# Kernel tuning notes

Measured on AMD Instinct MI355X. Metric: run time of the kernel, lower is better.

Reference implementation:

```python
import jax, jax.numpy as jnp
import numpy as np

B, Q, H, NH, HD = 2, 1024, 2048, 16, 128
QKV_ALPHA = 1e-4   # W8A8B8O8Linear output scale (a)
QKV_BETA = 1.0     # W8A8B8O8Linear bias scale (b)
QK_SCALE = 1e-4    # BMM_S8T_S8N_F32T dequant scale
PV_SCALE = 2e-3    # BMM_S8T_S8N_S8T output scale
DENSE_ALPHA = 1e-5 # W8A8BFP32OFP32Linear dequant scale
INV_NORM = 1.0 / (HD ** 0.5)


def setup_inputs() -> dict:
    key = jax.random.key(0)
    ks = jax.random.split(key, 8)
    hidden_states = jax.random.randint(ks[0], (B, Q, H), -128, 128, dtype=jnp.int32)  # int8 activations
    residual = jax.random.normal(ks[1], (B, Q, H), dtype=jnp.float32)
    alibi = jax.random.normal(ks[2], (B * NH, 1, Q), dtype=jnp.float32) * 0.1
    causal = jnp.triu(jnp.ones((Q, Q), dtype=bool), k=1)  # True = masked (future positions)
    attention_mask = jnp.broadcast_to(causal[None, None], (B, 1, Q, Q))
    w_qkv = jax.random.randint(ks[3], (3 * H, H), -128, 128, dtype=jnp.int32)   # int8 weight
    b_qkv = jax.random.randint(ks[4], (3 * H,), -128, 128, dtype=jnp.int32)     # int8 bias
    w_dense = jax.random.randint(ks[5], (H, H), -128, 128, dtype=jnp.int32)     # int8 weight
    b_dense = jax.random.normal(ks[6], (H,), dtype=jnp.float32)                 # fp32 bias
    return dict(hidden_states=hidden_states, residual=residual, alibi=alibi,
                attention_mask=attention_mask, w_qkv=w_qkv, b_qkv=b_qkv,
                w_dense=w_dense, b_dense=b_dense)


def _quant_i8(x_f32):
    return jnp.clip(jnp.round(x_f32), -128, 127).astype(jnp.int32)


def reference(hidden_states, residual, alibi, attention_mask, w_qkv, b_qkv, w_dense, b_dense):
    # --- W8A8B8O8 fused QKV linear: int8 in, int8 out ---
    acc = jnp.einsum('bqh,oh->bqo', hidden_states, w_qkv)  # exact int32 accumulation
    fused_qkv = _quant_i8(acc.astype(jnp.float32) * QKV_ALPHA + b_qkv.astype(jnp.float32) * QKV_BETA)
    # _split_heads: [B,Q,3H] -> [B,Q,NH,3,HD]
    qkv = fused_qkv.reshape(B, Q, NH, 3, HD)
    q = qkv[..., 0, :].transpose(0, 2, 1, 3).reshape(B * NH, Q, HD)
    k = qkv[..., 1, :].transpose(0, 2, 1, 3).reshape(B * NH, Q, HD)
    v = qkv[..., 2, :].transpose(0, 2, 1, 3).reshape(B * NH, Q, HD)
    # --- BMM_S8T_S8N_F32T: int8 q @ k^T -> fp32 * scale, plus alibi bias ---
    scores_i32 = jnp.einsum('nqd,nkd->nqk', q, k)  # [B*NH,Q,KV] int32
    matmul_result = alibi * 1.0 + scores_i32.astype(jnp.float32) * QK_SCALE * INV_NORM
    attention_scores = matmul_result.reshape(B, NH, Q, Q)
    # masked softmax (True = masked)
    attn_weights = jnp.where(attention_mask, jnp.finfo(jnp.float32).min, attention_scores)
    attention_probs = jax.nn.softmax(attn_weights, axis=-1)
    # quantize probs to int8 with scale 1/127 (BMM_S8T_S8N_S8T A-side)
    p_i8 = _quant_i8(attention_probs * 127.0).reshape(B * NH, Q, Q)
    # --- BMM_S8T_S8N_S8T: int8 probs @ int8 v -> int8 context ---
    ctx_acc = jnp.einsum('nqk,nkd->nqd', p_i8, v)  # int32
    ctx_i8 = _quant_i8(ctx_acc.astype(jnp.float32) * PV_SCALE)
    # _merge_heads: [B*NH,Q,HD] -> [B,Q,H]
    ctx = ctx_i8.reshape(B, NH, Q, HD).transpose(0, 2, 1, 3).reshape(B, Q, H)
    # --- W8A8BFP32OFP32 dense: int8 in, fp32 out ---
    dense_acc = jnp.einsum('bqh,oh->bqo', ctx, w_dense)
    output = dense_acc.astype(jnp.float32) * DENSE_ALPHA + b_dense + residual
    return output
```

## Files before the change

### kernel.cpp

```cpp
#include <hip/hip_runtime.h>
#include <stdint.h>

typedef int i32x4 __attribute__((ext_vector_type(4)));

#define DEV __device__ __forceinline__

DEV void glds16(const void* g, void* l) {
  __builtin_amdgcn_global_load_lds(
      (const __attribute__((address_space(1))) void*)g,
      (__attribute__((address_space(3))) void*)l, 16, 0, 0);
}

DEV int clampi8(float f) {
  int v = (int)rintf(f);
  return v < -128 ? -128 : (v > 127 ? 127 : v);
}

__global__ void pack_kernel(const int* __restrict__ src, int8_t* __restrict__ dst, int n4) {
  int i = blockIdx.x * blockDim.x + threadIdx.x;
  if (i < n4) {
    int4 v = ((const int4*)src)[i];
    char4 c;
    c.x = (char)v.x; c.y = (char)v.y; c.z = (char)v.z; c.w = (char)v.w;
    ((char4*)dst)[i] = c;
  }
}

template<int K>
DEV void gemm_core(const int8_t* __restrict__ A, const int8_t* __restrict__ B,
                   int row0, int col0, i32x4 acc[4][4], char* lA, char* lB,
                   int l, int w, int wm, int wn) {
  const int lr = l & 15, lg = l >> 4;
  for (int k0 = 0; k0 < K; k0 += 64) {
    __syncthreads();
#pragma unroll
    for (int t = 0; t < 2; ++t) {
      const int mb = w * 2 + t;
      glds16(A + (size_t)(row0 + mb * 16 + lr) * K + k0 + lg * 16, lA + mb * 1024);
      glds16(B + (size_t)(col0 + mb * 16 + lr) * K + k0 + lg * 16, lB + mb * 1024);
    }
    __syncthreads();
    i32x4 a[4], b[4];
#pragma unroll
    for (int i = 0; i < 4; ++i) a[i] = *(const i32x4*)(lA + ((wm * 4 + i) * 64 + l) * 16);
#pragma unroll
    for (int j = 0; j < 4; ++j) b[j] = *(const i32x4*)(lB + ((wn * 4 + j) * 64 + l) * 16);
#pragma unroll
    for (int i = 0; i < 4; ++i)
#pragma unroll
      for (int j = 0; j < 4; ++j)
        acc[i][j] = __builtin_amdgcn_mfma_i32_16x16x64_i8(a[i], b[j], acc[i][j], 0, 0, 0);
  }
}

__global__ __launch_bounds__(256) void qkv_kernel(
    const int8_t* __restrict__ hs8, const int8_t* __restrict__ w8,
    const int* __restrict__ bq, int8_t* __restrict__ qb, int8_t* __restrict__ kb,
    int8_t* __restrict__ vT) {
  __shared__ __align__(16) char lA[8192];
  __shared__ __align__(16) char lB[8192];
  const int l = threadIdx.x & 63, w = threadIdx.x >> 6;
  const int wm = w >> 1, wn = w & 1;
  const int lr = l & 15, lg = l >> 4;
  const int row0 = blockIdx.y * 128, col0 = blockIdx.x * 128;
  i32x4 acc[4][4] = {};
  gemm_core<2048>(hs8, w8, row0, col0, acc, lA, lB, l, w, wm, wn);
#pragma unroll
  for (int j = 0; j < 4; ++j) {
    const int col = col0 + (wn * 4 + j) * 16 + lr;
    const float bias = (float)bq[col];
    const int nh = col / 384, rem = col - nh * 384;
    const int s = rem >> 7, d = rem & 127;
#pragma unroll
    for (int i = 0; i < 4; ++i) {
#pragma unroll
      for (int r = 0; r < 4; ++r) {
        const int row = row0 + (wm * 4 + i) * 16 + lg * 4 + r;
        const int bb = row >> 10, qpos = row & 1023;
        const int n = bb * 16 + nh;
        const int8_t c = (int8_t)clampi8((float)acc[i][j][r] * 1e-4f + bias);
        if (s == 0)      qb[((size_t)n << 17) + (qpos << 7) + d] = c;
        else if (s == 1) kb[((size_t)n << 17) + (qpos << 7) + d] = c;
        else             vT[((size_t)n << 17) + (d << 10) + qpos] = c;
      }
    }
  }
}

__global__ __launch_bounds__(256) void attn_kernel(
    const int8_t* __restrict__ qb, const int8_t* __restrict__ kb,
    const int8_t* __restrict__ vT, const float* __restrict__ alibi,
    int8_t* __restrict__ ctx) {
  __shared__ __align__(16) char lQ[16384];
  __shared__ __align__(16) char lK[16384];
  __shared__ __align__(16) char lV[16384];
  __shared__ __align__(16) char lP[128 * 144];
  const int n = blockIdx.x, qt = blockIdx.y;
  const int l = threadIdx.x & 63, w = threadIdx.x >> 6;
  const int lr = l & 15, lg = l >> 4;
  const int row0 = qt * 128;
  const int8_t* Qh = qb + ((size_t)n << 17);
  const int8_t* Kh = kb + ((size_t)n << 17);
  const int8_t* Vh = vT + ((size_t)n << 17);
  const float* al = alibi + n * 1024;

#pragma unroll
  for (int e0 = 0; e0 < 4; ++e0) {
    const int e = w * 4 + e0, ks = e >> 3, mb = e & 7;
    glds16(Qh + (size_t)(row0 + mb * 16 + lr) * 128 + ks * 64 + lg * 16, lQ + e * 1024);
  }
  __syncthreads();
  i32x4 qa[2][2];
#pragma unroll
  for (int t = 0; t < 2; ++t)
#pragma unroll
    for (int ks = 0; ks < 2; ++ks)
      qa[t][ks] = *(const i32x4*)(lQ + (ks * 8 + w * 2 + t) * 1024 + l * 16);

  float mrow[2][4], srow[2][4];
#pragma unroll
  for (int t = 0; t < 2; ++t)
#pragma unroll
    for (int r = 0; r < 4; ++r) { mrow[t][r] = -INFINITY; srow[t][r] = 0.f; }

  for (int kt = 0; kt <= qt; ++kt) {
    __syncthreads();
#pragma unroll
    for (int e0 = 0; e0 < 4; ++e0) {
      const int e = w * 4 + e0, ks = e >> 3, mb = e & 7;
      glds16(Kh + (size_t)(kt * 128 + mb * 16 + lr) * 128 + ks * 64 + lg * 16, lK + e * 1024);
    }
    __syncthreads();
    float sf[2][8][4];
#pragma unroll
    for (int nf = 0; nf < 8; ++nf) {
      const i32x4 bk0 = *(const i32x4*)(lK + nf * 1024 + l * 16);
      const i32x4 bk1 = *(const i32x4*)(lK + (8 + nf) * 1024 + l * 16);
      const int col = kt * 128 + nf * 16 + lr;
      const float av = al[col];
#pragma unroll
      for (int t = 0; t < 2; ++t) {
        i32x4 sa = {0, 0, 0, 0};
        sa = __builtin_amdgcn_mfma_i32_16x16x64_i8(qa[t][0], bk0, sa, 0, 0, 0);
        sa = __builtin_amdgcn_mfma_i32_16x16x64_i8(qa[t][1], bk1, sa, 0, 0, 0);
#pragma unroll
        for (int r = 0; r < 4; ++r) {
          const int rowg = row0 + (w * 2 + t) * 16 + lg * 4 + r;
          sf[t][nf][r] = (col <= rowg)
              ? av + ((float)sa[r] * 1e-4f) * 0.08838834764831843f
              : -INFINITY;
        }
      }
    }
#pragma unroll
    for (int t = 0; t < 2; ++t)
#pragma unroll
      for (int r = 0; r < 4; ++r) {
        float tm = sf[t][0][r];
#pragma unroll
        for (int nf = 1; nf < 8; ++nf) tm = fmaxf(tm, sf[t][nf][r]);
#pragma unroll
        for (int o = 1; o < 16; o <<= 1) tm = fmaxf(tm, __shfl_xor(tm, o));
        const float mn = fmaxf(mrow[t][r], tm);
        float es = 0.f;
#pragma unroll
        for (int nf = 0; nf < 8; ++nf) es += expf(sf[t][nf][r] - mn);
#pragma unroll
        for (int o = 1; o < 16; o <<= 1) es += __shfl_xor(es, o);
        srow[t][r] = srow[t][r] * expf(mrow[t][r] - mn) + es;
        mrow[t][r] = mn;
      }
  }

  i32x4 pacc[2][8] = {};
  for (int kt = 0; kt <= qt; ++kt) {
    __syncthreads();
#pragma unroll
    for (int e0 = 0; e0 < 4; ++e0) {
      const int e = w * 4 + e0, ks = e >> 3, mb = e & 7;
      glds16(Kh + (size_t)(kt * 128 + mb * 16 + lr) * 128 + ks * 64 + lg * 16, lK + e * 1024);
      glds16(Vh + (size_t)(mb * 16 + lr) * 1024 + kt * 128 + ks * 64 + lg * 16, lV + e * 1024);
    }
    __syncthreads();
#pragma unroll
    for (int nf = 0; nf < 8; ++nf) {
      const i32x4 bk0 = *(const i32x4*)(lK + nf * 1024 + l * 16);
      const i32x4 bk1 = *(const i32x4*)(lK + (8 + nf) * 1024 + l * 16);
      const int col = kt * 128 + nf * 16 + lr;
      const float av = al[col];
#pragma unroll
      for (int t = 0; t < 2; ++t) {
        i32x4 sa = {0, 0, 0, 0};
        sa = __builtin_amdgcn_mfma_i32_16x16x64_i8(qa[t][0], bk0, sa, 0, 0, 0);
        sa = __builtin_amdgcn_mfma_i32_16x16x64_i8(qa[t][1], bk1, sa, 0, 0, 0);
#pragma unroll
        for (int r = 0; r < 4; ++r) {
          const int rowl = (w * 2 + t) * 16 + lg * 4 + r;
          const int rowg = row0 + rowl;
          int p = 0;
          if (col <= rowg) {
            const float s = av + ((float)sa[r] * 1e-4f) * 0.08838834764831843f;
            p = (int)rintf(expf(s - mrow[t][r]) / srow[t][r] * 127.0f);
          }
          lP[rowl * 144 + nf * 16 + lr] = (char)p;
        }
      }
    }
    __syncthreads();
#pragma unroll
    for (int t = 0; t < 2; ++t) {
      const int rowl = (w * 2 + t) * 16 + lr;
      const i32x4 pa0 = *(const i32x4*)(lP + rowl * 144 + lg * 16);
      const i32x4 pa1 = *(const i32x4*)(lP + rowl * 144 + 64 + lg * 16);
#pragma unroll
      for (int nf = 0; nf < 8; ++nf) {
        const i32x4 vb0 = *(const i32x4*)(lV + nf * 1024 + l * 16);
        const i32x4 vb1 = *(const i32x4*)(lV + (8 + nf) * 1024 + l * 16);
        pacc[t][nf] = __builtin_amdgcn_mfma_i32_16x16x64_i8(pa0, vb0, pacc[t][nf], 0, 0, 0);
        pacc[t][nf] = __builtin_amdgcn_mfma_i32_16x16x64_i8(pa1, vb1, pacc[t][nf], 0, 0, 0);
      }
    }
  }
  const int bb = n >> 4, nh = n & 15;
#pragma unroll
  for (int t = 0; t < 2; ++t)
#pragma unroll
    for (int nf = 0; nf < 8; ++nf)
#pragma unroll
      for (int r = 0; r < 4; ++r) {
        const int qpos = row0 + (w * 2 + t) * 16 + lg * 4 + r;
        const int d = nf * 16 + lr;
        ctx[((size_t)(bb * 1024 + qpos)) * 2048 + nh * 128 + d] =
            (int8_t)clampi8((float)pacc[t][nf][r] * 2e-3f);
      }
}

__global__ __launch_bounds__(256) void dense_kernel(
    const int8_t* __restrict__ c8, const int8_t* __restrict__ w8,
    const float* __restrict__ bd, const float* __restrict__ res,
    float* __restrict__ out) {
  __shared__ __align__(16) char lA[8192];
  __shared__ __align__(16) char lB[8192];
  const int l = threadIdx.x & 63, w = threadIdx.x >> 6;
  const int wm = w >> 1, wn = w & 1;
  const int lr = l & 15, lg = l >> 4;
  const int row0 = blockIdx.y * 128, col0 = blockIdx.x * 128;
  i32x4 acc[4][4] = {};
  gemm_core<2048>(c8, w8, row0, col0, acc, lA, lB, l, w, wm, wn);
#pragma unroll
  for (int j = 0; j < 4; ++j) {
    const int col = col0 + (wn * 4 + j) * 16 + lr;
    const float bias = bd[col];
#pragma unroll
    for (int i = 0; i < 4; ++i) {
#pragma unroll
      for (int r = 0; r < 4; ++r) {
        const int row = row0 + (wm * 4 + i) * 16 + lg * 4 + r;
        const size_t o = (size_t)row * 2048 + col;
        out[o] = (float)acc[i][j][r] * 1e-5f + bias + res[o];
      }
    }
  }
}

extern "C" void kernel_launch(void* const* d_in, const int* in_sizes, int n_in,
                              void* d_out, int out_size, void* d_ws, size_t ws_size,
                              hipStream_t stream) {
  const int* hs = (const int*)d_in[0];
  const float* res = (const float*)d_in[1];
  const float* alibi = (const float*)d_in[2];
  const int* wqkv = (const int*)d_in[4];
  const int* bqkv = (const int*)d_in[5];
  const int* wd = (const int*)d_in[6];
  const float* bd = (const float*)d_in[7];
  float* out = (float*)d_out;
  char* ws = (char*)d_ws;

  int8_t* hs8   = (int8_t*)(ws + 0);
  int8_t* wqkv8 = (int8_t*)(ws + 4194304);
  int8_t* wd8   = (int8_t*)(ws + 16777216);
  int8_t* q8b   = (int8_t*)(ws + 20971520);
  int8_t* k8b   = (int8_t*)(ws + 25165824);
  int8_t* vT8   = (int8_t*)(ws + 29360128);
  int8_t* ctx8  = (int8_t*)(ws + 33554432);

  pack_kernel<<<4096, 256, 0, stream>>>(hs, hs8, 1048576);
  pack_kernel<<<12288, 256, 0, stream>>>(wqkv, wqkv8, 3145728);
  pack_kernel<<<4096, 256, 0, stream>>>(wd, wd8, 1048576);
  qkv_kernel<<<dim3(48, 16), 256, 0, stream>>>(hs8, wqkv8, bqkv, q8b, k8b, vT8);
  attn_kernel<<<dim3(32, 8), 256, 0, stream>>>(q8b, k8b, vT8, alibi, ctx8);
  dense_kernel<<<dim3(16, 16), 256, 0, stream>>>(ctx8, wd8, bd, res, out);
}
```

Baseline: 210.8 us.

## Split attention into parallel per-tile stats pass and split-K PV pass with reduction

Replaces the single attention kernel, whose blocks ran two serial passes over the causal K tiles, with three kernels. The first computes per-(q-tile, k-tile) row max and exp-sum in parallel over all triangular tile pairs. The second merges those stats and runs the PV pass, splitting long query tiles into two K ranges that write int32 partials to slabs. A final kernel sums the partials and quantizes them. This aims to remove load imbalance and the serial stats pass, and it also switches to fast __expf. The cost is extra launches and global traffic for stats and slabs, which reuse workspace areas that held the packed inputs.

```diff
diff --git a/kernel.cpp b/kernel.cpp
--- a/kernel.cpp
+++ b/kernel.cpp
@@ -87,15 +87,93 @@
   }
 }
 
-__global__ __launch_bounds__(256) void attn_kernel(
+__global__ __launch_bounds__(256) void attn_stats_kernel(
+    const int8_t* __restrict__ qb, const int8_t* __restrict__ kb,
+    const float* __restrict__ alibi, float* __restrict__ stats) {
+  __shared__ __align__(16) char lQ[16384];
+  __shared__ __align__(16) char lK[16384];
+  const int n = blockIdx.y;
+  const int tri = blockIdx.x;
+  int qt = 0;
+  while ((qt + 1) * (qt + 2) / 2 <= tri) ++qt;
+  const int kt = tri - qt * (qt + 1) / 2;
+  const int l = threadIdx.x & 63, w = threadIdx.x >> 6;
+  const int lr = l & 15, lg = l >> 4;
+  const int row0 = qt * 128;
+  const int8_t* Qh = qb + ((size_t)n << 17);
+  const int8_t* Kh = kb + ((size_t)n << 17);
+  const float* al = alibi + n * 1024;
+
+#pragma unroll
+  for (int e0 = 0; e0 < 4; ++e0) {
+    const int e = w * 4 + e0, ks = e >> 3, mb = e & 7;
+    glds16(Qh + (size_t)(row0 + mb * 16 + lr) * 128 + ks * 64 + lg * 16, lQ + e * 1024);
+    glds16(Kh + (size_t)(kt * 128 + mb * 16 + lr) * 128 + ks * 64 + lg * 16, lK + e * 1024);
+  }
+  __syncthreads();
+  i32x4 qa[2][2];
+#pragma unroll
+  for (int t = 0; t < 2; ++t)
+#pragma unroll
+    for (int ks = 0; ks < 2; ++ks)
+      qa[t][ks] = *(const i32x4*)(lQ + (ks * 8 + w * 2 + t) * 1024 + l * 16);
+
+  float sf[2][8][4];
+#pragma unroll
+  for (int nf = 0; nf < 8; ++nf) {
+    const i32x4 bk0 = *(const i32x4*)(lK + nf * 1024 + l * 16);
+    const i32x4 bk1 = *(const i32x4*)(lK + (8 + nf) * 1024 + l * 16);
+    const int col = kt * 128 + nf * 16 + lr;
+    const float av = al[col];
+#pragma unroll
+    for (int t = 0; t < 2; ++t) {
+      i32x4 sa = {0, 0, 0, 0};
+      sa = __builtin_amdgcn_mfma_i32_16x16x64_i8(qa[t][0], bk0, sa, 0, 0, 0);
+      sa = __builtin_amdgcn_mfma_i32_16x16x64_i8(qa[t][1], bk1, sa, 0, 0, 0);
+#pragma unroll
+      for (int r = 0; r < 4; ++r) {
+        const int rowg = row0 + (w * 2 + t) * 16 + lg * 4 + r;
+        sf[t][nf][r] = (col <= rowg)
+            ? av + ((float)sa[r] * 1e-4f) * 0.08838834764831843f
+            : -INFINITY;
+      }
+    }
+  }
+#pragma unroll
+  for (int t = 0; t < 2; ++t)
+#pragma unroll
+    for (int r = 0; r < 4; ++r) {
+      float tm = sf[t][0][r];
+#pragma unroll
+      for (int nf = 1; nf < 8; ++nf) tm = fmaxf(tm, sf[t][nf][r]);
+#pragma unroll
+      for (int o = 1; o < 16; o <<= 1) tm = fmaxf(tm, __shfl_xor(tm, o));
+      float es = 0.f;
+#pragma unroll
+      for (int nf = 0; nf < 8; ++nf) es += __expf(sf[t][nf][r] - tm);
+#pragma unroll
+      for (int o = 1; o < 16; o <<= 1) es += __shfl_xor(es, o);
+      if (lr == 0) {
+        const int rowl = (w * 2 + t) * 16 + lg * 4 + r;
+        float2* st = (float2*)stats;
+        st[((n * 8 + qt) * 8 + kt) * 128 + rowl] = make_float2(tm, es);
+      }
+    }
+}
+
+__global__ __launch_bounds__(256) void attn_pv_kernel(
     const int8_t* __restrict__ qb, const int8_t* __restrict__ kb,
     const int8_t* __restrict__ vT, const float* __restrict__ alibi,
-    int8_t* __restrict__ ctx) {
+    const float* __restrict__ stats, int* __restrict__ slab0,
+    int* __restrict__ slab1, int8_t* __restrict__ ctx) {
   __shared__ __align__(16) char lQ[16384];
   __shared__ __align__(16) char lK[16384];
   __shared__ __align__(16) char lV[16384];
   __shared__ __align__(16) char lP[128 * 144];
-  const int n = blockIdx.x, qt = blockIdx.y;
+  const int n = blockIdx.y, gi = blockIdx.x;
+  int qt, g, kt0, kt1;
+  if (gi < 4) { qt = gi; g = 0; kt0 = 0; kt1 = qt + 1; }
+  else { const int p = gi - 4; qt = 4 + (p >> 1); g = p & 1; kt0 = g ? 4 : 0; kt1 = g ? qt + 1 : 4; }
   const int l = threadIdx.x & 63, w = threadIdx.x >> 6;
   const int lr = l & 15, lg = l >> 4;
   const int row0 = qt * 128;
@@ -118,62 +196,25 @@
       qa[t][ks] = *(const i32x4*)(lQ + (ks * 8 + w * 2 + t) * 1024 + l * 16);
 
   float mrow[2][4], srow[2][4];
+  const float2* st = (const float2*)stats;
 #pragma unroll
   for (int t = 0; t < 2; ++t)
 #pragma unroll
-    for (int r = 0; r < 4; ++r) { mrow[t][r] = -INFINITY; srow[t][r] = 0.f; }
-
-  for (int kt = 0; kt <= qt; ++kt) {
-    __syncthreads();
-#pragma unroll
-    for (int e0 = 0; e0 < 4; ++e0) {
-      const int e = w * 4 + e0, ks = e >> 3, mb = e & 7;
-      glds16(Kh + (size_t)(kt * 128 + mb * 16 + lr) * 128 + ks * 64 + lg * 16, lK + e * 1024);
-    }
-    __syncthreads();
-    float sf[2][8][4];
-#pragma unroll
-    for (int nf = 0; nf < 8; ++nf) {
-      const i32x4 bk0 = *(const i32x4*)(lK + nf * 1024 + l * 16);
-      const i32x4 bk1 = *(const i32x4*)(lK + (8 + nf) * 1024 + l * 16);
-      const int col = kt * 128 + nf * 16 + lr;
-      const float av = al[col];
-#pragma unroll
-      for (int t = 0; t < 2; ++t) {
-        i32x4 sa = {0, 0, 0, 0};
-        sa = __builtin_amdgcn_mfma_i32_16x16x64_i8(qa[t][0], bk0, sa, 0, 0, 0);
-        sa = __builtin_amdgcn_mfma_i32_16x16x64_i8(qa[t][1], bk1, sa, 0, 0, 0);
-#pragma unroll
-        for (int r = 0; r < 4; ++r) {
-          const int rowg = row0 + (w * 2 + t) * 16 + lg * 4 + r;
-          sf[t][nf][r] = (col <= rowg)
-              ? av + ((float)sa[r] * 1e-4f) * 0.08838834764831843f
-              : -INFINITY;
-        }
-      }
-    }
-#pragma unroll
-    for (int t = 0; t < 2; ++t)
-#pragma unroll
-      for (int r = 0; r < 4; ++r) {
-        float tm = sf[t][0][r];
-#pragma unroll
-        for (int nf = 1; nf < 8; ++nf) tm = fmaxf(tm, sf[t][nf][r]);
-#pragma unroll
-        for (int o = 1; o < 16; o <<= 1) tm = fmaxf(tm, __shfl_xor(tm, o));
-        const float mn = fmaxf(mrow[t][r], tm);
-        float es = 0.f;
-#pragma unroll
-        for (int nf = 0; nf < 8; ++nf) es += expf(sf[t][nf][r] - mn);
-#pragma unroll
-        for (int o = 1; o < 16; o <<= 1) es += __shfl_xor(es, o);
-        srow[t][r] = srow[t][r] * expf(mrow[t][r] - mn) + es;
-        mrow[t][r] = mn;
-      }
-  }
+    for (int r = 0; r < 4; ++r) {
+      const int rowl = (w * 2 + t) * 16 + lg * 4 + r;
+      const int base = ((n * 8 + qt) * 8) * 128 + rowl;
+      float m = -INFINITY;
+      for (int k2 = 0; k2 <= qt; ++k2) m = fmaxf(m, st[base + k2 * 128].x);
+      float s = 0.f;
+      for (int k2 = 0; k2 <= qt; ++k2) {
+        const float2 p = st[base + k2 * 128];
+        s += p.y * __expf(p.x - m);
+      }
+      mrow[t][r] = m; srow[t][r] = s;
+    }
 
   i32x4 pacc[2][8] = {};
-  for (int kt = 0; kt <= qt; ++kt) {
+  for (int kt = kt0; kt < kt1; ++kt) {
     __syncthreads();
 #pragma unroll
     for (int e0 = 0; e0 < 4; ++e0) {
@@ -200,7 +241,7 @@
           int p = 0;
           if (col <= rowg) {
             const float s = av + ((float)sa[r] * 1e-4f) * 0.08838834764831843f;
-            p = (int)rintf(expf(s - mrow[t][r]) / srow[t][r] * 127.0f);
+            p = (int)rintf(__expf(s - mrow[t][r]) / srow[t][r] * 127.0f);
           }
           lP[rowl * 144 + nf * 16 + lr] = (char)p;
         }
@@ -222,17 +263,48 @@
     }
   }
   const int bb = n >> 4, nh = n & 15;
-#pragma unroll
-  for (int t = 0; t < 2; ++t)
-#pragma unroll
-    for (int nf = 0; nf < 8; ++nf)
-#pragma unroll
-      for (int r = 0; r < 4; ++r) {
-        const int qpos = row0 + (w * 2 + t) * 16 + lg * 4 + r;
-        const int d = nf * 16 + lr;
-        ctx[((size_t)(bb * 1024 + qpos)) * 2048 + nh * 128 + d] =
-            (int8_t)clampi8((float)pacc[t][nf][r] * 2e-3f);
-      }
+  if (qt < 4) {
+#pragma unroll
+    for (int t = 0; t < 2; ++t)
+#pragma unroll
+      for (int nf = 0; nf < 8; ++nf)
+#pragma unroll
+        for (int r = 0; r < 4; ++r) {
+          const int qpos = row0 + (w * 2 + t) * 16 + lg * 4 + r;
+          const int d = nf * 16 + lr;
+          ctx[((size_t)(bb * 1024 + qpos)) * 2048 + nh * 128 + d] =
+              (int8_t)clampi8((float)pacc[t][nf][r] * 2e-3f);
+        }
+  } else {
+    int* slab = g ? slab1 : slab0;
+#pragma unroll
+    for (int t = 0; t < 2; ++t)
+#pragma unroll
+      for (int nf = 0; nf < 8; ++nf)
+#pragma unroll
+        for (int r = 0; r < 4; ++r) {
+          const int qpos = row0 + (w * 2 + t) * 16 + lg * 4 + r;
+          const int d = nf * 16 + lr;
+          slab[(size_t)(bb * 512 + qpos - 512) * 2048 + nh * 128 + d] = pacc[t][nf][r];
+        }
+  }
+}
+
+__global__ void ctx_reduce_kernel(const int* __restrict__ slab0,
+                                  const int* __restrict__ slab1,
+                                  int8_t* __restrict__ ctx) {
+  const int i = blockIdx.x * blockDim.x + threadIdx.x;
+  const int4 a = ((const int4*)slab0)[i];
+  const int4 b = ((const int4*)slab1)[i];
+  const int elem0 = i * 4;
+  const int r512 = elem0 >> 11, col = elem0 & 2047;
+  const int bb = r512 >> 9, qpos = 512 + (r512 & 511);
+  char4 c;
+  c.x = (char)clampi8((float)(a.x + b.x) * 2e-3f);
+  c.y = (char)clampi8((float)(a.y + b.y) * 2e-3f);
+  c.z = (char)clampi8((float)(a.z + b.z) * 2e-3f);
+  c.w = (char)clampi8((float)(a.w + b.w) * 2e-3f);
+  ((char4*)ctx)[((size_t)(bb * 1024 + qpos) * 2048 + col) >> 2] = c;
 }
 
 __global__ __launch_bounds__(256) void dense_kernel(
@@ -278,16 +350,22 @@
 
   int8_t* hs8   = (int8_t*)(ws + 0);
   int8_t* wqkv8 = (int8_t*)(ws + 4194304);
+  int*    slab0 = (int*)(ws + 0);
+  int*    slab1 = (int*)(ws + 8388608);
   int8_t* wd8   = (int8_t*)(ws + 16777216);
   int8_t* q8b   = (int8_t*)(ws + 20971520);
   int8_t* k8b   = (int8_t*)(ws + 25165824);
   int8_t* vT8   = (int8_t*)(ws + 29360128);
   int8_t* ctx8  = (int8_t*)(ws + 33554432);
+  float*  stats = (float*)(ws + 37748736);
 
   pack_kernel<<<4096, 256, 0, stream>>>(hs, hs8, 1048576);
   pack_kernel<<<12288, 256, 0, stream>>>(wqkv, wqkv8, 3145728);
   pack_kernel<<<4096, 256, 0, stream>>>(wd, wd8, 1048576);
   qkv_kernel<<<dim3(48, 16), 256, 0, stream>>>(hs8, wqkv8, bqkv, q8b, k8b, vT8);
-  attn_kernel<<<dim3(32, 8), 256, 0, stream>>>(q8b, k8b, vT8, alibi, ctx8);
+  attn_stats_kernel<<<dim3(36, 32), 256, 0, stream>>>(q8b, k8b, alibi, stats);
+  attn_pv_kernel<<<dim3(12, 32), 256, 0, stream>>>(q8b, k8b, vT8, alibi, stats,
+                                                   slab0, slab1, ctx8);
+  ctx_reduce_kernel<<<2048, 256, 0, stream>>>(slab0, slab1, ctx8);
   dense_kernel<<<dim3(16, 16), 256, 0, stream>>>(ctx8, wd8, bd, res, out);
 }
```

Result: faster. 189.5 us (-10.1%).
